# Optimization experiments

Hardware: AMD Instinct MI355X
Metric: run time of the kernel (lower is better)

The kernel has to match this reference:

```python
import jax, jax.numpy as jnp
import numpy as np

N_NODES = 50000
N_EDGES = 640000
D = 128      # node feature dim
ED = 128     # edge feature dim
H = 128      # MLP hidden dim


def _glorot(key, shape):
    fan_in = shape[0]
    return jax.random.normal(key, shape, jnp.float32) * (1.0 / np.sqrt(fan_in))


def setup_inputs() -> dict:
    key = jax.random.key(0)
    ks = jax.random.split(key, 12)
    x = jax.random.normal(ks[0], (N_NODES, D), jnp.float32)
    edge_index = jax.random.randint(ks[1], (2, N_EDGES), 0, N_NODES, jnp.int64)
    edge_attr = jax.random.normal(ks[2], (N_EDGES, ED), jnp.float32)
    # edge_model: MLP on concat([src, dest, edge_attr]) -> ED
    We1 = _glorot(ks[3], (2 * D + ED, H)); be1 = jnp.zeros((H,), jnp.float32)
    We2 = _glorot(ks[4], (H, ED));         be2 = jnp.zeros((ED,), jnp.float32)
    # node_model: MLP on concat([x, scatter_mean(edge_attr, row)]) -> D
    Wn1 = _glorot(ks[5], (D + ED, H));     bn1 = jnp.zeros((H,), jnp.float32)
    Wn2 = _glorot(ks[6], (H, D));          bn2 = jnp.zeros((D,), jnp.float32)
    return {"x": x, "edge_index": edge_index, "edge_attr": edge_attr,
            "We1": We1, "be1": be1, "We2": We2, "be2": be2,
            "Wn1": Wn1, "bn1": bn1, "Wn2": Wn2, "bn2": bn2}


def reference(x, edge_index, edge_attr, We1, be1, We2, be2, Wn1, bn1, Wn2, bn2):
    row = edge_index[0]  # source / aggregation target, [E]
    col = edge_index[1]  # destination, [E]
    # edge_model(x[row], x[col], edge_attr): concat -> 2-layer ReLU MLP
    e_in = jnp.concatenate([x[row], x[col], edge_attr], axis=1)  # [E, 2D+ED]
    edge_out = jax.nn.relu(e_in @ We1 + be1) @ We2 + be2          # [E, ED]
    # node_model: scatter-mean of edge messages onto row nodes
    agg = jax.ops.segment_sum(edge_out, row, num_segments=N_NODES)         # [N, ED]
    cnt = jax.ops.segment_sum(jnp.ones((edge_out.shape[0], 1), x.dtype),
                              row, num_segments=N_NODES)                    # [N, 1]
    mean = agg / jnp.maximum(cnt, 1.0)
    n_in = jnp.concatenate([x, mean], axis=1)                     # [N, D+ED]
    x_out = jax.nn.relu(n_in @ Wn1 + bn1) @ Wn2 + bn2             # [N, D]
    return (x_out, edge_out)
```

## Files before the change

kernel.cpp:

```cpp
#include <hip/hip_runtime.h>
#include <stdint.h>


#define E_EDGES 640000
#define N_NODES 50000
#define DIM 128

typedef unsigned short u16;
typedef unsigned int u32x4 __attribute__((ext_vector_type(4)));
typedef float f32x4 __attribute__((ext_vector_type(4)));
typedef float f32x2 __attribute__((ext_vector_type(2)));
typedef short s16x8 __attribute__((ext_vector_type(8)));
union U16 { u32x4 u; s16x8 s; u16 h[8]; };

__device__ __forceinline__ float b2f(u16 u) {
  union { unsigned i; float f; } v; v.i = ((unsigned)u) << 16; return v.f;
}
__device__ __forceinline__ u16 f2b(float f) {
  union { float f; unsigned u; } v; v.f = f;
  unsigned r = v.u + 0x7FFFu + ((v.u >> 16) & 1u);
  return (u16)(r >> 16);
}
__device__ __forceinline__ float ldf(const void* p, long long i, int isF32) {
  return isF32 ? ((const float*)p)[i] : b2f(((const u16*)p)[i]);
}

__global__ void detect_kernel(const void* x, const void* ei, int* flags) {
  __shared__ int sBig, sNz;
  if (threadIdx.x == 0) { sBig = 0; sNz = 0; }
  __syncthreads();
  const u16* xu = (const u16*)x;
  const int* ew = (const int*)ei;
  int big = 0, nz = 0;
  for (int i = threadIdx.x; i < 4096; i += 256) {
    u16 u = xu[2 * i];
    if (((u >> 7) & 0xFF) >= 0x90) big = 1;
    if (ew[2 * i + 1] != 0) nz = 1;
  }
  if (big) atomicOr(&sBig, 1);
  if (nz) atomicOr(&sNz, 1);
  __syncthreads();
  if (threadIdx.x == 0) { flags[0] = sBig; flags[1] = sNz ? 0 : 1; }
}

__global__ void normalize_idx(const void* ei, const int* __restrict__ flags,
                              int* __restrict__ out) {
  int i = blockIdx.x * 256 + threadIdx.x;
  if (flags[1]) out[i] = (int)((const long long*)ei)[i];
  else          out[i] = ((const int*)ei)[i];
}

__global__ void prep_weights(const void* We1, const void* be1, const void* We2,
                             const void* be2, const void* Wn1, const void* bn1,
                             const void* Wn2, const void* bn2,
                             const int* __restrict__ flags,
                             u16* __restrict__ WT1, u16* __restrict__ WT2,
                             u16* __restrict__ WnT1, u16* __restrict__ WnT2,
                             float* __restrict__ biasf) {
  const int isF32 = flags[0];
  int tid = blockIdx.x * 256 + threadIdx.x;
  if (tid < 384 * 128) { int k = tid >> 7, n = tid & 127; WT1 [n * 384 + k] = f2b(ldf(We1, tid, isF32)); }
  if (tid < 128 * 128) { int k = tid >> 7, n = tid & 127; WT2 [n * 128 + k] = f2b(ldf(We2, tid, isF32)); }
  if (tid < 256 * 128) { int k = tid >> 7, n = tid & 127; WnT1[n * 256 + k] = f2b(ldf(Wn1, tid, isF32)); }
  if (tid < 128 * 128) { int k = tid >> 7, n = tid & 127; WnT2[n * 128 + k] = f2b(ldf(Wn2, tid, isF32)); }
  if (tid < 128) {
    biasf[tid]       = ldf(be1, tid, isF32);
    biasf[128 + tid] = ldf(be2, tid, isF32);
    biasf[256 + tid] = ldf(bn1, tid, isF32);
    biasf[384 + tid] = ldf(bn2, tid, isF32);
  }
}

__global__ void convert_x(const void* x, const int* __restrict__ flags,
                          u16* __restrict__ xb) {
  int i = blockIdx.x * 256 + threadIdx.x;
  xb[i] = flags[0] ? f2b(((const float*)x)[i]) : ((const u16*)x)[i];
}

__global__ void hist_kernel(const int* __restrict__ ei,
                            int* __restrict__ ecnt) {
  const int e = blockIdx.x * 256 + threadIdx.x;
  atomicAdd(&ecnt[ei[e]], 1);
}

#define SCAN_CHUNK 196
__global__ __launch_bounds__(256) void scan_kernel(
    const int* __restrict__ ecnt, int* __restrict__ rowstart) {
  __shared__ int sums[256];
  __shared__ int pref[257];
  const int t = threadIdx.x;
  const int base = t * SCAN_CHUNK;
  int s = 0;
  for (int i = 0; i < SCAN_CHUNK; ++i) {
    const int idx = base + i;
    if (idx < N_NODES) s += ecnt[idx];
  }
  sums[t] = s;
  __syncthreads();
  if (t == 0) {
    int run = 0;
    for (int i = 0; i < 256; ++i) { pref[i] = run; run += sums[i]; }
    pref[256] = run;
  }
  __syncthreads();
  int run = pref[t];
  for (int i = 0; i < SCAN_CHUNK; ++i) {
    const int idx = base + i;
    if (idx < N_NODES) { rowstart[idx] = run; run += ecnt[idx]; }
  }
  if (t == 0) rowstart[N_NODES] = pref[256];
}

__global__ void scatter_kernel(const int* __restrict__ ei,
                               const int* __restrict__ rowstart,
                               int* __restrict__ cursor,
                               int* __restrict__ perm) {
  const int e = blockIdx.x * 256 + threadIdx.x;
  const int r = ei[e];
  const int pos = rowstart[r] + atomicAdd(&cursor[r], 1);
  perm[pos] = e;
}

__global__ __launch_bounds__(256) void edge_kernel(
    const u16* __restrict__ xb, const int* __restrict__ ei, const void* ea,
    const u16* __restrict__ WT1, const u16* __restrict__ WT2,
    const float* __restrict__ biasf, const int* __restrict__ flags,
    void* d_out) {
  __shared__ u16 h[4][32 * 136];
  const int isF32 = flags[0];
  const int wid = threadIdx.x >> 6, lane = threadIdx.x & 63;
  const int lm = lane & 15, quad = lane >> 4;
  const int ebase = (blockIdx.x * 4 + wid) * 32;

  const int e0 = ebase + lm, e1 = ebase + 16 + lm;
  const int row0 = ei[e0], col0 = ei[E_EDGES + e0];
  const int row1 = ei[e1], col1 = ei[E_EDGES + e1];

  const f32x4 fz = {0.f, 0.f, 0.f, 0.f};
  f32x4 acc[2][8];
#pragma unroll
  for (int mt = 0; mt < 2; ++mt)
#pragma unroll
    for (int t = 0; t < 8; ++t) acc[mt][t] = fz;

#pragma unroll
  for (int ks = 0; ks < 12; ++ks) {
    const int k0 = ks * 32 + quad * 8;
    U16 a0, a1;
    if (k0 < 256) {
      const u16 *p0, *p1;
      if (k0 < 128) { p0 = xb + (size_t)row0 * DIM + k0;         p1 = xb + (size_t)row1 * DIM + k0; }
      else          { p0 = xb + (size_t)col0 * DIM + (k0 - 128); p1 = xb + (size_t)col1 * DIM + (k0 - 128); }
      a0.u = *(const u32x4*)p0;
      a1.u = *(const u32x4*)p1;
    } else {
      const int off = k0 - 256;
      if (isF32) {
        const float* q0 = (const float*)ea + (size_t)e0 * DIM + off;
        const float* q1 = (const float*)ea + (size_t)e1 * DIM + off;
        f32x4 lo0 = *(const f32x4*)q0, hi0 = *(const f32x4*)(q0 + 4);
        f32x4 lo1 = *(const f32x4*)q1, hi1 = *(const f32x4*)(q1 + 4);
#pragma unroll
        for (int j = 0; j < 4; ++j) {
          a0.h[j] = f2b(lo0[j]); a0.h[4 + j] = f2b(hi0[j]);
          a1.h[j] = f2b(lo1[j]); a1.h[4 + j] = f2b(hi1[j]);
        }
      } else {
        const u16* q0 = (const u16*)ea + (size_t)e0 * DIM + off;
        const u16* q1 = (const u16*)ea + (size_t)e1 * DIM + off;
        a0.u = *(const u32x4*)q0;
        a1.u = *(const u32x4*)q1;
      }
    }
#pragma unroll
    for (int t = 0; t < 8; ++t) {
      U16 b; b.u = *(const u32x4*)(WT1 + (t * 16 + lm) * 384 + k0);
      acc[0][t] = __builtin_amdgcn_mfma_f32_16x16x32_bf16(a0.s, b.s, acc[0][t], 0, 0, 0);
      acc[1][t] = __builtin_amdgcn_mfma_f32_16x16x32_bf16(a1.s, b.s, acc[1][t], 0, 0, 0);
    }
  }

  u16* hw = h[wid];
#pragma unroll
  for (int t = 0; t < 8; ++t) {
    const int n = t * 16 + lm;
    const float bias = biasf[n];
#pragma unroll
    for (int mt = 0; mt < 2; ++mt)
#pragma unroll
      for (int r = 0; r < 4; ++r) {
        float v = acc[mt][t][r] + bias;
        v = v > 0.f ? v : 0.f;
        hw[(mt * 16 + quad * 4 + r) * 136 + n] = f2b(v);
      }
  }
  __syncthreads();

  f32x4 acc2[2][8];
#pragma unroll
  for (int mt = 0; mt < 2; ++mt)
#pragma unroll
    for (int t = 0; t < 8; ++t) acc2[mt][t] = fz;

#pragma unroll
  for (int ks = 0; ks < 4; ++ks) {
    const int k0 = ks * 32 + quad * 8;
    U16 a0, a1;
    a0.u = *(const u32x4*)(hw + lm * 136 + k0);
    a1.u = *(const u32x4*)(hw + (16 + lm) * 136 + k0);
#pragma unroll
    for (int t = 0; t < 8; ++t) {
      U16 b; b.u = *(const u32x4*)(WT2 + (t * 16 + lm) * 128 + k0);
      acc2[0][t] = __builtin_amdgcn_mfma_f32_16x16x32_bf16(a0.s, b.s, acc2[0][t], 0, 0, 0);
      acc2[1][t] = __builtin_amdgcn_mfma_f32_16x16x32_bf16(a1.s, b.s, acc2[1][t], 0, 0, 0);
    }
  }

  float* eoutf = (float*)d_out + (size_t)N_NODES * DIM;
  u16*   eoutb = (u16*)d_out   + (size_t)N_NODES * DIM;

#pragma unroll
  for (int t = 0; t < 8; ++t) {
    const int n = t * 16 + lm;
    const float bias = biasf[128 + n];
#pragma unroll
    for (int mt = 0; mt < 2; ++mt)
#pragma unroll
      for (int r = 0; r < 4; ++r) {
        float v = acc2[mt][t][r] + bias;
        const size_t e = (size_t)(ebase + mt * 16 + quad * 4 + r);
        if (isF32) eoutf[e * DIM + n] = v;
        else       eoutb[e * DIM + n] = f2b(v);
      }
  }
}

__global__ __launch_bounds__(256) void agg_kernel(
    const void* d_out, const int* __restrict__ rowstart,
    const int* __restrict__ perm, const int* __restrict__ flags,
    u16* __restrict__ meanb) {
  const int isF32 = flags[0];
  const int wid = threadIdx.x >> 6, lane = threadIdx.x & 63;
  const int node = blockIdx.x * 4 + wid;
  if (node >= N_NODES) return;
  const int beg = rowstart[node], end = rowstart[node + 1];
  float s0 = 0.f, s1 = 0.f;
  if (isF32) {
    const float* base = (const float*)d_out + (size_t)N_NODES * DIM;
    int j = beg;
    for (; j + 2 <= end; j += 2) {
      const int ea0 = perm[j], ea1 = perm[j + 1];
      const f32x2 v0 = *(const f32x2*)(base + (size_t)ea0 * DIM + lane * 2);
      const f32x2 v1 = *(const f32x2*)(base + (size_t)ea1 * DIM + lane * 2);
      s0 += v0.x + v1.x; s1 += v0.y + v1.y;
    }
    if (j < end) {
      const int ea0 = perm[j];
      const f32x2 v0 = *(const f32x2*)(base + (size_t)ea0 * DIM + lane * 2);
      s0 += v0.x; s1 += v0.y;
    }
  } else {
    const u16* base = (const u16*)d_out + (size_t)N_NODES * DIM;
    int j = beg;
    for (; j + 2 <= end; j += 2) {
      const int ea0 = perm[j], ea1 = perm[j + 1];
      const unsigned v0 = *(const unsigned*)(base + (size_t)ea0 * DIM + lane * 2);
      const unsigned v1 = *(const unsigned*)(base + (size_t)ea1 * DIM + lane * 2);
      s0 += b2f((u16)(v0 & 0xFFFF)) + b2f((u16)(v1 & 0xFFFF));
      s1 += b2f((u16)(v0 >> 16)) + b2f((u16)(v1 >> 16));
    }
    if (j < end) {
      const int ea0 = perm[j];
      const unsigned v0 = *(const unsigned*)(base + (size_t)ea0 * DIM + lane * 2);
      s0 += b2f((u16)(v0 & 0xFFFF));
      s1 += b2f((u16)(v0 >> 16));
    }
  }
  const float inv = 1.0f / fmaxf((float)(end - beg), 1.0f);
  const unsigned out = ((unsigned)f2b(s1 * inv) << 16) | (unsigned)f2b(s0 * inv);
  *(unsigned*)(meanb + (size_t)node * DIM + lane * 2) = out;
}

__global__ __launch_bounds__(256) void node_kernel(
    const u16* __restrict__ xb, const u16* __restrict__ meanb,
    const u16* __restrict__ WnT1, const u16* __restrict__ WnT2,
    const float* __restrict__ biasf, const int* __restrict__ flags,
    void* d_out) {
  __shared__ u16 h[4][32 * 136];
  const int isF32 = flags[0];
  const int wid = threadIdx.x >> 6, lane = threadIdx.x & 63;
  const int lm = lane & 15, quad = lane >> 4;
  const int nbase = (blockIdx.x * 4 + wid) * 32;

  int nd0 = nbase + lm;      if (nd0 > N_NODES - 1) nd0 = N_NODES - 1;
  int nd1 = nbase + 16 + lm; if (nd1 > N_NODES - 1) nd1 = N_NODES - 1;

  const f32x4 fz = {0.f, 0.f, 0.f, 0.f};
  f32x4 acc[2][8];
#pragma unroll
  for (int mt = 0; mt < 2; ++mt)
#pragma unroll
    for (int t = 0; t < 8; ++t) acc[mt][t] = fz;

#pragma unroll
  for (int ks = 0; ks < 8; ++ks) {
    const int k0 = ks * 32 + quad * 8;
    const u16 *p0, *p1;
    if (k0 < 128) { p0 = xb + (size_t)nd0 * DIM + k0;            p1 = xb + (size_t)nd1 * DIM + k0; }
    else          { p0 = meanb + (size_t)nd0 * DIM + (k0 - 128); p1 = meanb + (size_t)nd1 * DIM + (k0 - 128); }
    U16 a0, a1;
    a0.u = *(const u32x4*)p0;
    a1.u = *(const u32x4*)p1;
#pragma unroll
    for (int t = 0; t < 8; ++t) {
      U16 b; b.u = *(const u32x4*)(WnT1 + (t * 16 + lm) * 256 + k0);
      acc[0][t] = __builtin_amdgcn_mfma_f32_16x16x32_bf16(a0.s, b.s, acc[0][t], 0, 0, 0);
      acc[1][t] = __builtin_amdgcn_mfma_f32_16x16x32_bf16(a1.s, b.s, acc[1][t], 0, 0, 0);
    }
  }

  u16* hw = h[wid];
#pragma unroll
  for (int t = 0; t < 8; ++t) {
    const int n = t * 16 + lm;
    const float bias = biasf[256 + n];
#pragma unroll
    for (int mt = 0; mt < 2; ++mt)
#pragma unroll
      for (int r = 0; r < 4; ++r) {
        float v = acc[mt][t][r] + bias;
        v = v > 0.f ? v : 0.f;
        hw[(mt * 16 + quad * 4 + r) * 136 + n] = f2b(v);
      }
  }
  __syncthreads();

  f32x4 acc2[2][8];
#pragma unroll
  for (int mt = 0; mt < 2; ++mt)
#pragma unroll
    for (int t = 0; t < 8; ++t) acc2[mt][t] = fz;

#pragma unroll
  for (int ks = 0; ks < 4; ++ks) {
    const int k0 = ks * 32 + quad * 8;
    U16 a0, a1;
    a0.u = *(const u32x4*)(hw + lm * 136 + k0);
    a1.u = *(const u32x4*)(hw + (16 + lm) * 136 + k0);
#pragma unroll
    for (int t = 0; t < 8; ++t) {
      U16 b; b.u = *(const u32x4*)(WnT2 + (t * 16 + lm) * 128 + k0);
      acc2[0][t] = __builtin_amdgcn_mfma_f32_16x16x32_bf16(a0.s, b.s, acc2[0][t], 0, 0, 0);
      acc2[1][t] = __builtin_amdgcn_mfma_f32_16x16x32_bf16(a1.s, b.s, acc2[1][t], 0, 0, 0);
    }
  }

  float* xoutf = (float*)d_out;
  u16*   xoutb = (u16*)d_out;
#pragma unroll
  for (int t = 0; t < 8; ++t) {
    const int n = t * 16 + lm;
    const float bias = biasf[384 + n];
#pragma unroll
    for (int mt = 0; mt < 2; ++mt)
#pragma unroll
      for (int r = 0; r < 4; ++r) {
        const int node = nbase + mt * 16 + quad * 4 + r;
        if (node < N_NODES) {
          float v = acc2[mt][t][r] + bias;
          if (isF32) xoutf[(size_t)node * DIM + n] = v;
          else       xoutb[(size_t)node * DIM + n] = f2b(v);
        }
      }
  }
}

extern "C" void kernel_launch(void* const* d_in, const int* in_sizes, int n_in,
                              void* d_out, int out_size, void* d_ws, size_t ws_size,
                              hipStream_t stream) {
  const void* x   = d_in[0];
  const void* ei  = d_in[1];
  const void* ea  = d_in[2];
  const void* We1 = d_in[3]; const void* be1 = d_in[4];
  const void* We2 = d_in[5]; const void* be2 = d_in[6];
  const void* Wn1 = d_in[7]; const void* bn1 = d_in[8];
  const void* Wn2 = d_in[9]; const void* bn2 = d_in[10];

  char* ws = (char*)d_ws;
  int*   flags    = (int*)(ws + 0);
  float* biasf    = (float*)(ws + 256);
  u16*   WT1      = (u16*)(ws + 4096);
  u16*   WT2      = (u16*)(ws + 102400);
  u16*   WnT1     = (u16*)(ws + 135168);
  u16*   WnT2     = (u16*)(ws + 200704);
  int*   eidx32   = (int*)(ws + 233472);
  int*   ecnt     = (int*)(ws + 5353472);
  int*   cursor   = (int*)(ws + 5553472);
  int*   rowstart = (int*)(ws + 5753472);
  int*   perm     = (int*)(ws + 5953536);
  u16*   meanb    = (u16*)(ws + 8513536);
  u16*   xb       = (u16*)(ws + 21313536);

  hipMemsetAsync(ws + 5353472, 0, 400000, stream);

  detect_kernel<<<1, 256, 0, stream>>>(x, ei, flags);
  normalize_idx<<<2 * E_EDGES / 256, 256, 0, stream>>>(ei, flags, eidx32);
  prep_weights<<<192, 256, 0, stream>>>(We1, be1, We2, be2, Wn1, bn1, Wn2, bn2,
                                        flags, WT1, WT2, WnT1, WnT2, biasf);
  convert_x<<<N_NODES * DIM / 256, 256, 0, stream>>>(x, flags, xb);

  hist_kernel<<<E_EDGES / 256, 256, 0, stream>>>(eidx32, ecnt);
  scan_kernel<<<1, 256, 0, stream>>>(ecnt, rowstart);
  scatter_kernel<<<E_EDGES / 256, 256, 0, stream>>>(eidx32, rowstart, cursor, perm);

  edge_kernel<<<E_EDGES / 128, 256, 0, stream>>>(xb, eidx32, ea, WT1, WT2,
                                                 biasf, flags, d_out);
  agg_kernel<<<N_NODES / 4, 256, 0, stream>>>(d_out, rowstart, perm, flags, meanb);
  node_kernel<<<(N_NODES + 127) / 128, 256, 0, stream>>>(xb, meanb, WnT1, WnT2,
                                                         biasf, flags, d_out);
}
```

Before: 1.177 ms.

## Prefetch MLP inputs upfront, fuse histogram into index normalize, shrink node tiles

The edge kernel now loads all twelve gathered A fragments (src, dst and edge_attr) into registers before the MFMA loop, so global latency overlaps instead of stalling each k-step. It also gains a launch_bounds occupancy hint. The histogram atomic is folded into the index-normalization kernel, removing one launch and a reread of indices. The aggregation loop is unrolled by four to keep more gathers in flight, and the node kernel uses 16-node tiles per wave with register-prefetched inputs to get more blocks. Register pressure rises in the edge kernel, and the launch bound may force spills.

New measurement: 1.171 ms. About the same (-0.5%).

```diff
diff --git a/kernel.cpp b/kernel.cpp
--- a/kernel.cpp
+++ b/kernel.cpp
@@ -43,11 +43,14 @@
   if (threadIdx.x == 0) { flags[0] = sBig; flags[1] = sNz ? 0 : 1; }
 }
 
-__global__ void normalize_idx(const void* ei, const int* __restrict__ flags,
-                              int* __restrict__ out) {
+__global__ void normalize_hist(const void* ei, const int* __restrict__ flags,
+                               int* __restrict__ out, int* __restrict__ ecnt) {
   int i = blockIdx.x * 256 + threadIdx.x;
-  if (flags[1]) out[i] = (int)((const long long*)ei)[i];
-  else          out[i] = ((const int*)ei)[i];
+  int v;
+  if (flags[1]) v = (int)((const long long*)ei)[i];
+  else          v = ((const int*)ei)[i];
+  out[i] = v;
+  if (i < E_EDGES) atomicAdd(&ecnt[v], 1);
 }
 
 __global__ void prep_weights(const void* We1, const void* be1, const void* We2,
@@ -77,12 +80,6 @@
   xb[i] = flags[0] ? f2b(((const float*)x)[i]) : ((const u16*)x)[i];
 }
 
-__global__ void hist_kernel(const int* __restrict__ ei,
-                            int* __restrict__ ecnt) {
-  const int e = blockIdx.x * 256 + threadIdx.x;
-  atomicAdd(&ecnt[ei[e]], 1);
-}
-
 #define SCAN_CHUNK 196
 __global__ __launch_bounds__(256) void scan_kernel(
     const int* __restrict__ ecnt, int* __restrict__ rowstart) {
@@ -121,7 +118,7 @@
   perm[pos] = e;
 }
 
-__global__ __launch_bounds__(256) void edge_kernel(
+__global__ __launch_bounds__(256, 2) void edge_kernel(
     const u16* __restrict__ xb, const int* __restrict__ ei, const void* ea,
     const u16* __restrict__ WT1, const u16* __restrict__ WT2,
     const float* __restrict__ biasf, const int* __restrict__ flags,
@@ -136,6 +133,50 @@
   const int row0 = ei[e0], col0 = ei[E_EDGES + e0];
   const int row1 = ei[e1], col1 = ei[E_EDGES + e1];
 
+  U16 A0[12], A1[12];
+  {
+    const u16* r0 = xb + (size_t)row0 * DIM;
+    const u16* r1 = xb + (size_t)row1 * DIM;
+    const u16* c0 = xb + (size_t)col0 * DIM;
+    const u16* c1 = xb + (size_t)col1 * DIM;
+#pragma unroll
+    for (int ks = 0; ks < 4; ++ks) {
+      const int k0 = ks * 32 + quad * 8;
+      A0[ks].u = *(const u32x4*)(r0 + k0);
+      A1[ks].u = *(const u32x4*)(r1 + k0);
+    }
+#pragma unroll
+    for (int ks = 4; ks < 8; ++ks) {
+      const int k0 = (ks - 4) * 32 + quad * 8;
+      A0[ks].u = *(const u32x4*)(c0 + k0);
+      A1[ks].u = *(const u32x4*)(c1 + k0);
+    }
+    if (isF32) {
+      const float* q0 = (const float*)ea + (size_t)e0 * DIM;
+      const float* q1 = (const float*)ea + (size_t)e1 * DIM;
+#pragma unroll
+      for (int ks = 8; ks < 12; ++ks) {
+        const int off = (ks - 8) * 32 + quad * 8;
+        f32x4 lo0 = *(const f32x4*)(q0 + off), hi0 = *(const f32x4*)(q0 + off + 4);
+        f32x4 lo1 = *(const f32x4*)(q1 + off), hi1 = *(const f32x4*)(q1 + off + 4);
+#pragma unroll
+        for (int j = 0; j < 4; ++j) {
+          A0[ks].h[j] = f2b(lo0[j]); A0[ks].h[4 + j] = f2b(hi0[j]);
+          A1[ks].h[j] = f2b(lo1[j]); A1[ks].h[4 + j] = f2b(hi1[j]);
+        }
+      }
+    } else {
+      const u16* q0 = (const u16*)ea + (size_t)e0 * DIM;
+      const u16* q1 = (const u16*)ea + (size_t)e1 * DIM;
+#pragma unroll
+      for (int ks = 8; ks < 12; ++ks) {
+        const int off = (ks - 8) * 32 + quad * 8;
+        A0[ks].u = *(const u32x4*)(q0 + off);
+        A1[ks].u = *(const u32x4*)(q1 + off);
+      }
+    }
+  }
+
   const f32x4 fz = {0.f, 0.f, 0.f, 0.f};
   f32x4 acc[2][8];
 #pragma unroll
@@ -146,37 +187,11 @@
 #pragma unroll
   for (int ks = 0; ks < 12; ++ks) {
     const int k0 = ks * 32 + quad * 8;
-    U16 a0, a1;
-    if (k0 < 256) {
-      const u16 *p0, *p1;
-      if (k0 < 128) { p0 = xb + (size_t)row0 * DIM + k0;         p1 = xb + (size_t)row1 * DIM + k0; }
-      else          { p0 = xb + (size_t)col0 * DIM + (k0 - 128); p1 = xb + (size_t)col1 * DIM + (k0 - 128); }
-      a0.u = *(const u32x4*)p0;
-      a1.u = *(const u32x4*)p1;
-    } else {
-      const int off = k0 - 256;
-      if (isF32) {
-        const float* q0 = (const float*)ea + (size_t)e0 * DIM + off;
-        const float* q1 = (const float*)ea + (size_t)e1 * DIM + off;
-        f32x4 lo0 = *(const f32x4*)q0, hi0 = *(const f32x4*)(q0 + 4);
-        f32x4 lo1 = *(const f32x4*)q1, hi1 = *(const f32x4*)(q1 + 4);
-#pragma unroll
-        for (int j = 0; j < 4; ++j) {
-          a0.h[j] = f2b(lo0[j]); a0.h[4 + j] = f2b(hi0[j]);
-          a1.h[j] = f2b(lo1[j]); a1.h[4 + j] = f2b(hi1[j]);
-        }
-      } else {
-        const u16* q0 = (const u16*)ea + (size_t)e0 * DIM + off;
-        const u16* q1 = (const u16*)ea + (size_t)e1 * DIM + off;
-        a0.u = *(const u32x4*)q0;
-        a1.u = *(const u32x4*)q1;
-      }
-    }
 #pragma unroll
     for (int t = 0; t < 8; ++t) {
       U16 b; b.u = *(const u32x4*)(WT1 + (t * 16 + lm) * 384 + k0);
-      acc[0][t] = __builtin_amdgcn_mfma_f32_16x16x32_bf16(a0.s, b.s, acc[0][t], 0, 0, 0);
-      acc[1][t] = __builtin_amdgcn_mfma_f32_16x16x32_bf16(a1.s, b.s, acc[1][t], 0, 0, 0);
+      acc[0][t] = __builtin_amdgcn_mfma_f32_16x16x32_bf16(A0[ks].s, b.s, acc[0][t], 0, 0, 0);
+      acc[1][t] = __builtin_amdgcn_mfma_f32_16x16x32_bf16(A1[ks].s, b.s, acc[1][t], 0, 0, 0);
     }
   }
 
@@ -248,30 +263,35 @@
   if (isF32) {
     const float* base = (const float*)d_out + (size_t)N_NODES * DIM;
     int j = beg;
-    for (; j + 2 <= end; j += 2) {
-      const int ea0 = perm[j], ea1 = perm[j + 1];
-      const f32x2 v0 = *(const f32x2*)(base + (size_t)ea0 * DIM + lane * 2);
-      const f32x2 v1 = *(const f32x2*)(base + (size_t)ea1 * DIM + lane * 2);
-      s0 += v0.x + v1.x; s1 += v0.y + v1.y;
-    }
-    if (j < end) {
-      const int ea0 = perm[j];
-      const f32x2 v0 = *(const f32x2*)(base + (size_t)ea0 * DIM + lane * 2);
+    for (; j + 4 <= end; j += 4) {
+      const int p0 = perm[j], p1 = perm[j + 1], p2 = perm[j + 2], p3 = perm[j + 3];
+      const f32x2 v0 = *(const f32x2*)(base + (size_t)p0 * DIM + lane * 2);
+      const f32x2 v1 = *(const f32x2*)(base + (size_t)p1 * DIM + lane * 2);
+      const f32x2 v2 = *(const f32x2*)(base + (size_t)p2 * DIM + lane * 2);
+      const f32x2 v3 = *(const f32x2*)(base + (size_t)p3 * DIM + lane * 2);
+      s0 += v0.x + v1.x + v2.x + v3.x;
+      s1 += v0.y + v1.y + v2.y + v3.y;
+    }
+    for (; j < end; ++j) {
+      const f32x2 v0 = *(const f32x2*)(base + (size_t)perm[j] * DIM + lane * 2);
       s0 += v0.x; s1 += v0.y;
     }
   } else {
     const u16* base = (const u16*)d_out + (size_t)N_NODES * DIM;
     int j = beg;
-    for (; j + 2 <= end; j += 2) {
-      const int ea0 = perm[j], ea1 = perm[j + 1];
-      const unsigned v0 = *(const unsigned*)(base + (size_t)ea0 * DIM + lane * 2);
-      const unsigned v1 = *(const unsigned*)(base + (size_t)ea1 * DIM + lane * 2);
-      s0 += b2f((u16)(v0 & 0xFFFF)) + b2f((u16)(v1 & 0xFFFF));
-      s1 += b2f((u16)(v0 >> 16)) + b2f((u16)(v1 >> 16));
-    }
-    if (j < end) {
-      const int ea0 = perm[j];
-      const unsigned v0 = *(const unsigned*)(base + (size_t)ea0 * DIM + lane * 2);
+    for (; j + 4 <= end; j += 4) {
+      const int p0 = perm[j], p1 = perm[j + 1], p2 = perm[j + 2], p3 = perm[j + 3];
+      const unsigned v0 = *(const unsigned*)(base + (size_t)p0 * DIM + lane * 2);
+      const unsigned v1 = *(const unsigned*)(base + (size_t)p1 * DIM + lane * 2);
+      const unsigned v2 = *(const unsigned*)(base + (size_t)p2 * DIM + lane * 2);
+      const unsigned v3 = *(const unsigned*)(base + (size_t)p3 * DIM + lane * 2);
+      s0 += b2f((u16)(v0 & 0xFFFF)) + b2f((u16)(v1 & 0xFFFF)) +
+            b2f((u16)(v2 & 0xFFFF)) + b2f((u16)(v3 & 0xFFFF));
+      s1 += b2f((u16)(v0 >> 16)) + b2f((u16)(v1 >> 16)) +
+            b2f((u16)(v2 >> 16)) + b2f((u16)(v3 >> 16));
+    }
+    for (; j < end; ++j) {
+      const unsigned v0 = *(const unsigned*)(base + (size_t)perm[j] * DIM + lane * 2);
       s0 += b2f((u16)(v0 & 0xFFFF));
       s1 += b2f((u16)(v0 >> 16));
     }
@@ -286,36 +306,38 @@
     const u16* __restrict__ WnT1, const u16* __restrict__ WnT2,
     const float* __restrict__ biasf, const int* __restrict__ flags,
     void* d_out) {
-  __shared__ u16 h[4][32 * 136];
+  __shared__ u16 h[4][16 * 136];
   const int isF32 = flags[0];
   const int wid = threadIdx.x >> 6, lane = threadIdx.x & 63;
   const int lm = lane & 15, quad = lane >> 4;
-  const int nbase = (blockIdx.x * 4 + wid) * 32;
-
-  int nd0 = nbase + lm;      if (nd0 > N_NODES - 1) nd0 = N_NODES - 1;
-  int nd1 = nbase + 16 + lm; if (nd1 > N_NODES - 1) nd1 = N_NODES - 1;
+  const int nbase = (blockIdx.x * 4 + wid) * 16;
+
+  int nd0 = nbase + lm; if (nd0 > N_NODES - 1) nd0 = N_NODES - 1;
+
+  U16 A0[8];
+  {
+    const u16* r0 = xb    + (size_t)nd0 * DIM;
+    const u16* m0 = meanb + (size_t)nd0 * DIM;
+#pragma unroll
+    for (int ks = 0; ks < 4; ++ks) {
+      const int k0 = ks * 32 + quad * 8;
+      A0[ks].u     = *(const u32x4*)(r0 + k0);
+      A0[ks + 4].u = *(const u32x4*)(m0 + k0);
+    }
+  }
 
   const f32x4 fz = {0.f, 0.f, 0.f, 0.f};
-  f32x4 acc[2][8];
-#pragma unroll
-  for (int mt = 0; mt < 2; ++mt)
-#pragma unroll
-    for (int t = 0; t < 8; ++t) acc[mt][t] = fz;
+  f32x4 acc[8];
+#pragma unroll
+  for (int t = 0; t < 8; ++t) acc[t] = fz;
 
 #pragma unroll
   for (int ks = 0; ks < 8; ++ks) {
     const int k0 = ks * 32 + quad * 8;
-    const u16 *p0, *p1;
-    if (k0 < 128) { p0 = xb + (size_t)nd0 * DIM + k0;            p1 = xb + (size_t)nd1 * DIM + k0; }
-    else          { p0 = meanb + (size_t)nd0 * DIM + (k0 - 128); p1 = meanb + (size_t)nd1 * DIM + (k0 - 128); }
-    U16 a0, a1;
-    a0.u = *(const u32x4*)p0;
-    a1.u = *(const u32x4*)p1;
 #pragma unroll
     for (int t = 0; t < 8; ++t) {
       U16 b; b.u = *(const u32x4*)(WnT1 + (t * 16 + lm) * 256 + k0);
-      acc[0][t] = __builtin_amdgcn_mfma_f32_16x16x32_bf16(a0.s, b.s, acc[0][t], 0, 0, 0);
-      acc[1][t] = __builtin_amdgcn_mfma_f32_16x16x32_bf16(a1.s, b.s, acc[1][t], 0, 0, 0);
+      acc[t] = __builtin_amdgcn_mfma_f32_16x16x32_bf16(A0[ks].s, b.s, acc[t], 0, 0, 0);
     }
   }
 
@@ -325,33 +347,27 @@
     const int n = t * 16 + lm;
     const float bias = biasf[256 + n];
 #pragma unroll
-    for (int mt = 0; mt < 2; ++mt)
-#pragma unroll
-      for (int r = 0; r < 4; ++r) {
-        float v = acc[mt][t][r] + bias;
-        v = v > 0.f ? v : 0.f;
-        hw[(mt * 16 + quad * 4 + r) * 136 + n] = f2b(v);
-      }
-  }
-  __syncthreads();
-
-  f32x4 acc2[2][8];
-#pragma unroll
-  for (int mt = 0; mt < 2; ++mt)
-#pragma unroll
-    for (int t = 0; t < 8; ++t) acc2[mt][t] = fz;
+    for (int r = 0; r < 4; ++r) {
+      float v = acc[t][r] + bias;
+      v = v > 0.f ? v : 0.f;
+      hw[(quad * 4 + r) * 136 + n] = f2b(v);
+    }
+  }
+  __syncthreads();
+
+  f32x4 acc2[8];
+#pragma unroll
+  for (int t = 0; t < 8; ++t) acc2[t] = fz;
 
 #pragma unroll
   for (int ks = 0; ks < 4; ++ks) {
     const int k0 = ks * 32 + quad * 8;
-    U16 a0, a1;
+    U16 a0;
     a0.u = *(const u32x4*)(hw + lm * 136 + k0);
-    a1.u = *(const u32x4*)(hw + (16 + lm) * 136 + k0);
 #pragma unroll
     for (int t = 0; t < 8; ++t) {
       U16 b; b.u = *(const u32x4*)(WnT2 + (t * 16 + lm) * 128 + k0);
-      acc2[0][t] = __builtin_amdgcn_mfma_f32_16x16x32_bf16(a0.s, b.s, acc2[0][t], 0, 0, 0);
-      acc2[1][t] = __builtin_amdgcn_mfma_f32_16x16x32_bf16(a1.s, b.s, acc2[1][t], 0, 0, 0);
+      acc2[t] = __builtin_amdgcn_mfma_f32_16x16x32_bf16(a0.s, b.s, acc2[t], 0, 0, 0);
     }
   }
 
@@ -362,16 +378,14 @@
     const int n = t * 16 + lm;
     const float bias = biasf[384 + n];
 #pragma unroll
-    for (int mt = 0; mt < 2; ++mt)
-#pragma unroll
-      for (int r = 0; r < 4; ++r) {
-        const int node = nbase + mt * 16 + quad * 4 + r;
-        if (node < N_NODES) {
-          float v = acc2[mt][t][r] + bias;
-          if (isF32) xoutf[(size_t)node * DIM + n] = v;
-          else       xoutb[(size_t)node * DIM + n] = f2b(v);
-        }
+    for (int r = 0; r < 4; ++r) {
+      const int node = nbase + quad * 4 + r;
+      if (node < N_NODES) {
+        float v = acc2[t][r] + bias;
+        if (isF32) xoutf[(size_t)node * DIM + n] = v;
+        else       xoutb[(size_t)node * DIM + n] = f2b(v);
       }
+    }
   }
 }
 
@@ -404,18 +418,17 @@
   hipMemsetAsync(ws + 5353472, 0, 400000, stream);
 
   detect_kernel<<<1, 256, 0, stream>>>(x, ei, flags);
-  normalize_idx<<<2 * E_EDGES / 256, 256, 0, stream>>>(ei, flags, eidx32);
+  normalize_hist<<<2 * E_EDGES / 256, 256, 0, stream>>>(ei, flags, eidx32, ecnt);
   prep_weights<<<192, 256, 0, stream>>>(We1, be1, We2, be2, Wn1, bn1, Wn2, bn2,
                                         flags, WT1, WT2, WnT1, WnT2, biasf);
   convert_x<<<N_NODES * DIM / 256, 256, 0, stream>>>(x, flags, xb);
 
-  hist_kernel<<<E_EDGES / 256, 256, 0, stream>>>(eidx32, ecnt);
   scan_kernel<<<1, 256, 0, stream>>>(ecnt, rowstart);
   scatter_kernel<<<E_EDGES / 256, 256, 0, stream>>>(eidx32, rowstart, cursor, perm);
 
   edge_kernel<<<E_EDGES / 128, 256, 0, stream>>>(xb, eidx32, ea, WT1, WT2,
                                                  biasf, flags, d_out);
   agg_kernel<<<N_NODES / 4, 256, 0, stream>>>(d_out, rowstart, perm, flags, meanb);
-  node_kernel<<<(N_NODES + 127) / 128, 256, 0, stream>>>(xb, meanb, WnT1, WnT2,
-                                                         biasf, flags, d_out);
-}
+  node_kernel<<<(N_NODES + 63) / 64, 256, 0, stream>>>(xb, meanb, WnT1, WnT2,
+                                                       biasf, flags, d_out);
+}
```
